# Performance work log

Hardware: AMD Instinct MI355X
Metric: run time of the kernel (lower is better)

The kernel has to match this reference:

```python
import jax, jax.numpy as jnp
import numpy as np

B, N, DIM, H, CH, M = 2, 65536, 256, 8, 32, 64
INNER = H * CH  # 256


def setup_inputs() -> dict:
    key = jax.random.key(0)
    ks = jax.random.split(key, 13)
    s = 0.02
    return {
        "x": jax.random.normal(ks[0], (B, N, DIM), dtype=jnp.float32),
        "W_fx": jax.random.normal(ks[1], (DIM, INNER), dtype=jnp.float32) * s,
        "b_fx": jnp.zeros((INNER,), dtype=jnp.float32),
        "W_x": jax.random.normal(ks[2], (DIM, INNER), dtype=jnp.float32) * s,
        "b_x": jnp.zeros((INNER,), dtype=jnp.float32),
        "W_slice": jax.random.normal(ks[3], (CH, M), dtype=jnp.float32) * s,
        "b_slice": jnp.zeros((M,), dtype=jnp.float32),
        "temperature": 0.5 * jnp.ones((1, H, 1, 1), dtype=jnp.float32),
        "W_q": jax.random.normal(ks[4], (CH, CH), dtype=jnp.float32) * s,
        "W_k": jax.random.normal(ks[5], (CH, CH), dtype=jnp.float32) * s,
        "W_v": jax.random.normal(ks[6], (CH, CH), dtype=jnp.float32) * s,
        "W_out": jax.random.normal(ks[7], (INNER, DIM), dtype=jnp.float32) * s,
        "b_out": jnp.zeros((DIM,), dtype=jnp.float32),
    }


def reference(x, W_fx, b_fx, W_x, b_x, W_slice, b_slice, temperature,
              W_q, W_k, W_v, W_out, b_out):
    b, n, _ = x.shape
    h, ch, m = H, CH, M
    # input projections -> [B, H, N, Ch]
    fx_mid = (x @ W_fx + b_fx).reshape(b, n, h, ch).transpose(0, 2, 1, 3)
    x_mid = (x @ W_x + b_x).reshape(b, n, h, ch).transpose(0, 2, 1, 3)
    # learned soft-slice weights: [B, H, N, M]
    temp = jnp.clip(temperature, 0.1, 5.0)
    logits = (x_mid @ W_slice + b_slice) / temp
    slice_weights = jax.nn.softmax(logits, axis=-1)
    slice_norm = slice_weights.sum(axis=2)  # [B, H, M]
    # aggregate N points into M slice tokens: [B, H, M, Ch]
    slice_token = jnp.einsum('bhnc,bhng->bhgc', fx_mid, slice_weights)
    slice_token = slice_token / (slice_norm + 1e-5)[:, :, :, None]
    # small attention among slice tokens
    q = slice_token @ W_q
    k = slice_token @ W_k
    v = slice_token @ W_v
    scale = ch ** (-0.5)
    attn = jax.nn.softmax(jnp.einsum('bhgc,bhkc->bhgk', q, k) * scale, axis=-1)
    out_slice = attn @ v  # [B, H, M, Ch]
    # scatter back to N points: [B, H, N, Ch] -> [B, N, H*Ch]
    out_x = jnp.einsum('bhgc,bhng->bhnc', out_slice, slice_weights)
    out_x = out_x.transpose(0, 2, 1, 3).reshape(b, n, h * ch)
    return out_x @ W_out + b_out
```

## Files before the change

kernel.cpp:

```cpp
#include <hip/hip_runtime.h>

#define N_ 65536

typedef unsigned int  uint32;
typedef unsigned short ushort;
typedef float  f32x4 __attribute__((ext_vector_type(4)));
typedef short  s16x8 __attribute__((ext_vector_type(8)));
typedef uint32 u32x2 __attribute__((ext_vector_type(2)));

__device__ __forceinline__ uint32 f2bf(float f){
  union{float f; uint32 i;} v; v.f=f;
  return (v.i + 0x7fffu + ((v.i>>16)&1u)) >> 16;
}
__device__ __forceinline__ float bfl(uint32 h){
  union{uint32 i; float f;} v; v.i = h<<16; return v.f;
}
__device__ __forceinline__ uint32 pk2(float a, float b){
  return f2bf(a) | (f2bf(b)<<16);
}
__device__ __forceinline__ f32x4 mfma16(s16x8 a, s16x8 b, f32x4 c){
  return __builtin_amdgcn_mfma_f32_16x16x32_bf16(a,b,c,0,0,0);
}

__global__ __launch_bounds__(256) void prep_kernel(
    const float* __restrict__ Wfx, const float* __restrict__ Wx,
    const float* __restrict__ Wsl, const float* __restrict__ bsl,
    const float* __restrict__ bx,  const float* __restrict__ temp,
    ushort* __restrict__ WlT, ushort* __restrict__ WfxT, float* __restrict__ blT)
{
  const int blk = blockIdx.x, t = threadIdx.x;
  if (blk < 512){
    const int m = blk, h = m>>6, mp = m&63;
    const float tmp = fminf(fmaxf(temp[h],0.1f),5.0f);
    float s = 0.f;
    #pragma unroll
    for (int cc=0; cc<32; cc++) s += Wx[t*256 + h*32+cc]*Wsl[cc*64+mp];
    WlT[m*256+t] = (ushort)f2bf(s/tmp);
    if (t==0){
      float bs = bsl[mp];
      for (int cc=0; cc<32; cc++) bs += bx[h*32+cc]*Wsl[cc*64+mp];
      blT[m] = bs/tmp;
    }
  } else {
    const int c = blk-512;
    WfxT[c*256+t] = (ushort)f2bf(Wfx[t*256+c]);
  }
}

__global__ __launch_bounds__(512, 2)
void k1a_kernel(
    const float* __restrict__ x,
    const ushort* __restrict__ WlT,
    const ushort* __restrict__ WfxT,
    const float* __restrict__ blT,
    const float* __restrict__ bfx,
    ushort* __restrict__ swg,
    float* __restrict__ stp,
    float* __restrict__ normp)
{
  __shared__ __align__(16) char smem[131072];
  const int t = threadIdx.x;
  const int w = t>>6, l = t&63, rg = l>>4, c16 = l&15;
  const int blk = blockIdx.x;
  const int tile0 = ((blk&127)<<3) + ((blk>>7)<<10);

  char* fxh = smem + (w<<12);
  char* swb = smem + 32768 + (w<<13);
  char* fxl = smem + 98304 + (w<<12);

  f32x4 pc[2][4];
  #pragma unroll
  for (int i=0;i<2;i++)
    #pragma unroll
    for (int j=0;j<4;j++) pc[i][j] = (f32x4){0.f,0.f,0.f,0.f};
  f32x4 nacc[4];
  #pragma unroll
  for (int i=0;i<4;i++) nacc[i] = (f32x4){0.f,0.f,0.f,0.f};

  f32x4 blv[4];
  #pragma unroll
  for (int m=0;m<4;m++) blv[m] = *(const f32x4*)(blT + (w<<6)+(m<<4)+(rg<<2));
  float bfv[2];
  #pragma unroll
  for (int c=0;c<2;c++) bfv[c] = bfx[(w<<5)+(c<<4)+c16];

  for (int it=0; it<8; ++it) {
    const int tile = tile0 + it;
    const long gn0 = (long)tile<<6;

    __syncthreads();
    {
      const float4* xs = (const float4*)(x + (gn0<<8));
      #pragma unroll
      for (int p=0;p<8;p++){
        const int f = t + (p<<9);
        const int row = f>>6, q = f&63;
        const float4 v = xs[f];
        u32x2 uu; uu.x = pk2(v.x, v.y); uu.y = pk2(v.z, v.w);
        *(u32x2*)(smem + (row<<9) + ((q<<3) ^ ((row&7)<<4))) = uu;
      }
    }
    __syncthreads();

    #pragma unroll
    for (int nf=0; nf<4; nf++){
      f32x4 accA[4];
      #pragma unroll
      for (int m=0;m<4;m++) accA[m] = (f32x4){0.f,0.f,0.f,0.f};
      #pragma unroll
      for (int kb=0;kb<8;kb++){
        s16x8 aW[4], bX;
        #pragma unroll
        for (int m=0;m<4;m++)
          aW[m] = *(const s16x8*)(WlT + (((w<<6)+(m<<4)+c16)<<8) + (kb<<5)+(rg<<3));
        {
          const int row = (nf<<4) | c16;
          bX = *(const s16x8*)(smem + (row<<9) + (((kb<<6)+(rg<<4)) ^ ((row&7)<<4)));
        }
        #pragma unroll
        for (int m=0;m<4;m++)
          accA[m] = mfma16(aW[m], bX, accA[m]);
      }
      {
        f32x4 v[4];
        float mx = -3.0e38f;
        #pragma unroll
        for (int m=0;m<4;m++){
          v[m] = accA[m] + blv[m];
          mx = fmaxf(mx, fmaxf(fmaxf(v[m].x, v[m].y), fmaxf(v[m].z, v[m].w)));
        }
        mx = fmaxf(mx, __shfl_xor(mx,16));
        mx = fmaxf(mx, __shfl_xor(mx,32));
        float s = 0.f;
        #pragma unroll
        for (int m=0;m<4;m++){
          v[m].x = __expf(v[m].x-mx); v[m].y = __expf(v[m].y-mx);
          v[m].z = __expf(v[m].z-mx); v[m].w = __expf(v[m].w-mx);
          s += v[m].x+v[m].y+v[m].z+v[m].w;
        }
        s += __shfl_xor(s,16);
        s += __shfl_xor(s,32);
        const float inv = 1.0f/s;
        const long gn = gn0 + (nf<<4) + c16;
        #pragma unroll
        for (int m=0;m<4;m++){
          f32x4 sv = v[m]*inv;
          nacc[m] += sv;
          u32x2 p; p.x = pk2(sv.x, sv.y); p.y = pk2(sv.z, sv.w);
          *(u32x2*)(swg + (gn<<9) + (w<<6)+(m<<4)+(rg<<2)) = p;
          const uint32 px = (uint32)__shfl_xor((int)p.x, 1);
          const uint32 py = (uint32)__shfl_xor((int)p.y, 1);
          const bool ev = ((c16&1)==0);
          const uint32 s0 = ev ? (uint32)p.x : py;
          const uint32 s1 = ev ? px : (uint32)p.y;
          const uint32 wA = (s0 & 0xffffu) | (s1<<16);
          const uint32 wB = (s0>>16) | (s1 & 0xffff0000u);
          const int rowA = (m<<4) + (rg<<2) + (ev?0:2);
          const int cbyt = ((nf<<4) + (c16 & ~1)) << 1;
          *(uint32*)(swb + ((rowA  )<<7) + (cbyt ^ (((rowA  )&7)<<4))) = wA;
          *(uint32*)(swb + ((rowA+1)<<7) + (cbyt ^ (((rowA+1)&7)<<4))) = wB;
        }
      }
    }

    u32x2 qkh[2][4];
    {
      f32x4 accB[4][2];
      #pragma unroll
      for (int r=0;r<4;r++)
        #pragma unroll
        for (int c=0;c<2;c++) accB[r][c] = (f32x4){0.f,0.f,0.f,0.f};
      #pragma unroll
      for (int kb=0;kb<8;kb++){
        s16x8 bW[2], aX[4];
        #pragma unroll
        for (int c=0;c<2;c++)
          bW[c] = *(const s16x8*)(WfxT + (((w<<5)+(c<<4)+c16)<<8) + (kb<<5)+(rg<<3));
        #pragma unroll
        for (int r=0;r<4;r++){
          const int row = (r<<4) | c16;
          aX[r] = *(const s16x8*)(smem + (row<<9) + (((kb<<6)+(rg<<4)) ^ ((row&7)<<4)));
        }
        #pragma unroll
        for (int r=0;r<4;r++)
          #pragma unroll
          for (int c=0;c<2;c++)
            accB[r][c] = mfma16(aX[r], bW[c], accB[r][c]);
      }
      #pragma unroll
      for (int r=0;r<4;r++)
        #pragma unroll
        for (int c=0;c<2;c++){
          const float v0 = accB[r][c].x+bfv[c], v1 = accB[r][c].y+bfv[c];
          const float v2 = accB[r][c].z+bfv[c], v3 = accB[r][c].w+bfv[c];
          const uint32 h0=f2bf(v0), h1=f2bf(v1), h2=f2bf(v2), h3=f2bf(v3);
          u32x2 ph; ph.x = h0|(h1<<16); ph.y = h2|(h3<<16);
          qkh[c][r] = ph;
          u32x2 pl;
          pl.x = f2bf(v0-bfl(h0)) | (f2bf(v1-bfl(h1))<<16);
          pl.y = f2bf(v2-bfl(h2)) | (f2bf(v3-bfl(h3))<<16);
          const int row = (c<<4) + c16;
          const int cby = ((r<<5) + (rg<<3)) ^ ((row&7)<<4);
          *(u32x2*)(fxl + (row<<7) + cby) = pl;
        }
    }
    __syncthreads();

    #pragma unroll
    for (int cf=0; cf<2; cf++)
      #pragma unroll
      for (int r=0; r<4; r++){
        const int row = (cf<<4) + c16;
        const int cby = ((r<<5) + (rg<<3)) ^ ((row&7)<<4);
        *(u32x2*)(fxh + (row<<7) + cby) = qkh[cf][r];
      }
    asm volatile("s_waitcnt lgkmcnt(0)" ::: "memory");
    __builtin_amdgcn_sched_barrier(0);

    #pragma unroll
    for (int kb2=0; kb2<2; kb2++){
      const int pby = (kb2<<6) + (rg<<4);
      s16x8 afh[2], afl[2], bfr[4];
      #pragma unroll
      for (int cf=0; cf<2; cf++){
        const int row = (cf<<4)+c16;
        const int o = pby ^ ((row&7)<<4);
        afh[cf] = *(const s16x8*)(fxh + (row<<7) + o);
        afl[cf] = *(const s16x8*)(fxl + (row<<7) + o);
      }
      #pragma unroll
      for (int mf=0; mf<4; mf++){
        const int row = (mf<<4)+c16;
        bfr[mf] = *(const s16x8*)(swb + (row<<7) + (pby ^ ((row&7)<<4)));
      }
      #pragma unroll
      for (int cf=0; cf<2; cf++)
        #pragma unroll
        for (int mf=0; mf<4; mf++){
          pc[cf][mf] = mfma16(afh[cf], bfr[mf], pc[cf][mf]);
          pc[cf][mf] = mfma16(afl[cf], bfr[mf], pc[cf][mf]);
        }
    }
  }

  #pragma unroll
  for (int m=0;m<4;m++){
    #pragma unroll
    for (int d=1; d<16; d<<=1){
      nacc[m].x += __shfl_xor(nacc[m].x, d);
      nacc[m].y += __shfl_xor(nacc[m].y, d);
      nacc[m].z += __shfl_xor(nacc[m].z, d);
      nacc[m].w += __shfl_xor(nacc[m].w, d);
    }
  }
  if (c16==0){
    #pragma unroll
    for (int m=0;m<4;m++)
      *(f32x4*)(normp + (((blk<<3)+w)<<6) + (m<<4) + (rg<<2)) = nacc[m];
  }
  const long sb = ((long)((blk<<3)+w))<<11;
  #pragma unroll
  for (int cf=0;cf<2;cf++)
    #pragma unroll
    for (int mf=0;mf<4;mf++)
      #pragma unroll
      for (int r=0;r<4;r++){
        const int cc = (cf<<4)+(rg<<2)+r;
        stp[sb + (cc<<6) + (mf<<4) + c16] = pc[cf][mf][r];
      }
}

__global__ __launch_bounds__(256) void k2a_kernel(float* __restrict__ stp, float* __restrict__ normp)
{
  const int gid = blockIdx.x;
  const int bh = gid>>3, grp = gid&7;
  const int b = bh>>3, h = bh&7;
  const int t = threadIdx.x;
  const int blk0 = (b<<7) + (grp<<4);
  f32x4 a0 = {0,0,0,0}, a1 = {0,0,0,0};
  for (int i=0;i<16;i++){
    const f32x4* p = (const f32x4*)(stp + ((((size_t)(blk0+i)<<3)+h)<<11) + ((size_t)t<<3));
    a0 += p[0]; a1 += p[1];
  }
  f32x4* q = (f32x4*)(stp + ((((size_t)blk0<<3)+h)<<11) + ((size_t)t<<3));
  q[0] = a0; q[1] = a1;
  if (t<8){
    f32x4 n0 = {0,0,0,0}, n1 = {0,0,0,0};
    for (int i=0;i<16;i++){
      const f32x4* p = (const f32x4*)(normp + (((blk0+i)<<3)+h)*64 + (t<<3));
      n0 += p[0]; n1 += p[1];
    }
    f32x4* qn = (f32x4*)(normp + ((blk0<<3)+h)*64 + (t<<3));
    qn[0] = n0; qn[1] = n1;
  }
}

__global__ __launch_bounds__(256) void k2b_kernel(
    const float* __restrict__ stp, const float* __restrict__ normp,
    const float* __restrict__ Wq, const float* __restrict__ Wk, const float* __restrict__ Wv,
    const float* __restrict__ Wout, ushort* __restrict__ OS2Th, ushort* __restrict__ OS2Tl)
{
  __shared__ float nrmL[64];
  __shared__ float tok[2048];
  __shared__ float qL[2048], kL[2048], vL[2048];
  __shared__ float sc[4096];
  __shared__ float osL[2048];
  const int bh = blockIdx.x; const int b = bh>>3, h = bh&7;
  const int t = threadIdx.x;

  if (t<64){
    float s = 0.f;
    for (int g=0; g<8; g++) s += normp[((((b<<7)+(g<<4))<<3)+h)*64 + t];
    nrmL[t] = s;
  }
  __syncthreads();
  {
    f32x4 a0 = {0,0,0,0}, a1 = {0,0,0,0};
    for (int g=0; g<8; g++){
      const f32x4* p = (const f32x4*)(stp + ((((size_t)((b<<7)+(g<<4))<<3)+h)<<11) + ((size_t)t<<3));
      a0 += p[0]; a1 += p[1];
    }
    const int c = t>>3, m0 = (t&7)<<3;
    #pragma unroll
    for (int j=0;j<4;j++) tok[(m0+j)*32 + c]   = a0[j] / (nrmL[m0+j]   + 1e-5f);
    #pragma unroll
    for (int j=0;j<4;j++) tok[(m0+4+j)*32 + c] = a1[j] / (nrmL[m0+4+j] + 1e-5f);
  }
  __syncthreads();

  const int g = t>>2, q4 = t&3;
  float aq[8]={0,0,0,0,0,0,0,0}, ak2[8]={0,0,0,0,0,0,0,0}, av[8]={0,0,0,0,0,0,0,0};
  for (int kk=0; kk<32; kk++){
    const float tv = tok[(g<<5)+kk];
    const int wo = kk*32 + (q4<<3);
    #pragma unroll
    for (int j=0;j<8;j++){
      aq[j]  = fmaf(tv, Wq[wo+j], aq[j]);
      ak2[j] = fmaf(tv, Wk[wo+j], ak2[j]);
      av[j]  = fmaf(tv, Wv[wo+j], av[j]);
    }
  }
  #pragma unroll
  for (int j=0;j<8;j++){
    qL[(g<<5)+(q4<<3)+j]=aq[j];
    kL[(g<<5)+(q4<<3)+j]=ak2[j];
    vL[(g<<5)+(q4<<3)+j]=av[j];
  }
  __syncthreads();

  const float scale = 0.17677669529663689f;
  float svv[16]; float mx = -3.0e38f;
  for (int mm=0;mm<16;mm++){
    const int m = (q4<<4)+mm;
    float s2 = 0.f;
    #pragma unroll
    for (int c=0;c<32;c++) s2 = fmaf(qL[(g<<5)+c], kL[(m<<5)+c], s2);
    s2 *= scale;
    svv[mm] = s2; mx = fmaxf(mx, s2);
  }
  mx = fmaxf(mx, __shfl_xor(mx,1));
  mx = fmaxf(mx, __shfl_xor(mx,2));
  float ssum = 0.f;
  for (int mm=0;mm<16;mm++){ svv[mm] = __expf(svv[mm]-mx); ssum += svv[mm]; }
  ssum += __shfl_xor(ssum,1); ssum += __shfl_xor(ssum,2);
  const float isum = 1.0f/ssum;
  for (int mm=0;mm<16;mm++) sc[(g<<6) + (q4<<4) + mm] = svv[mm]*isum;
  __syncthreads();

  float os[8]={0,0,0,0,0,0,0,0};
  for (int m=0;m<64;m++){
    const float a = sc[(g<<6)+m];
    const int vo = (m<<5)+(q4<<3);
    #pragma unroll
    for (int j=0;j<8;j++) os[j] = fmaf(a, vL[vo+j], os[j]);
  }
  #pragma unroll
  for (int j=0;j<8;j++) osL[(g<<5)+(q4<<3)+j] = os[j];
  __syncthreads();

  const int d = t;
  float wcol[32];
  #pragma unroll
  for (int c=0;c<32;c++) wcol[c] = Wout[(h*32+c)*256 + d];
  uint32* orh = (uint32*)(OS2Th + ((size_t)(b*256+d))*512 + h*64);
  uint32* orl = (uint32*)(OS2Tl + ((size_t)(b*256+d))*512 + h*64);
  #pragma unroll 4
  for (int g2=0; g2<32; g2++){
    float s0=0.f, s1=0.f;
    #pragma unroll
    for (int c=0;c<32;c++){
      s0 = fmaf(osL[((g2*2  )<<5)+c], wcol[c], s0);
      s1 = fmaf(osL[((g2*2+1)<<5)+c], wcol[c], s1);
    }
    const uint32 h0 = f2bf(s0), h1 = f2bf(s1);
    orh[g2] = h0 | (h1<<16);
    orl[g2] = f2bf(s0 - bfl(h0)) | (f2bf(s1 - bfl(h1)) << 16);
  }
}

__global__ __launch_bounds__(256) void k3_kernel(
    const ushort* __restrict__ swg,
    const ushort* __restrict__ OS2Th,
    const ushort* __restrict__ OS2Tl,
    const float* __restrict__ bout,
    float* __restrict__ out)
{
  const int t = threadIdx.x, w = t>>6, l = t&63, rg = l>>4, c16 = l&15;
  const int blk = blockIdx.x;
  const long gn0 = (long)blk<<7;
  const int b = blk>>9;
  f32x4 acc[8][4];
  #pragma unroll
  for (int r=0;r<8;r++)
    #pragma unroll
    for (int c=0;c<4;c++) acc[r][c] = (f32x4){0.f,0.f,0.f,0.f};
  const ushort* swp = swg + (gn0<<9);
  const long obb = (((long)(b<<8) + (w<<6))<<9);
  for (int kb=0;kb<16;kb++){
    s16x8 aS[8];
    #pragma unroll
    for (int r=0;r<8;r++)
      aS[r] = *(const s16x8*)(swp + ((long)((r<<4)+c16)<<9) + (kb<<5)+(rg<<3));
    #pragma unroll
    for (int c=0;c<4;c++){
      const long ro = obb + ((long)((c<<4)+c16)<<9) + (kb<<5)+(rg<<3);
      const s16x8 bh = *(const s16x8*)(OS2Th + ro);
      const s16x8 bl = *(const s16x8*)(OS2Tl + ro);
      #pragma unroll
      for (int r=0;r<8;r++)
        acc[r][c] = mfma16(aS[r], bh, acc[r][c]);
      #pragma unroll
      for (int r=0;r<8;r++)
        acc[r][c] = mfma16(aS[r], bl, acc[r][c]);
    }
  }
  float bo[4];
  #pragma unroll
  for (int c=0;c<4;c++) bo[c] = bout[(w<<6)+(c<<4)+c16];
  #pragma unroll
  for (int r=0;r<8;r++)
    #pragma unroll
    for (int c=0;c<4;c++)
      #pragma unroll
      for (int rr=0;rr<4;rr++)
        out[((gn0 + (r<<4)+(rg<<2)+rr)<<8) + (w<<6)+(c<<4)+c16] = acc[r][c][rr] + bo[c];
}

extern "C" void kernel_launch(void* const* d_in, const int* in_sizes, int n_in,
                              void* d_out, int out_size, void* d_ws, size_t ws_size,
                              hipStream_t stream)
{
  const float* x     = (const float*)d_in[0];
  const float* Wfx   = (const float*)d_in[1];
  const float* bfx   = (const float*)d_in[2];
  const float* Wx    = (const float*)d_in[3];
  const float* bx    = (const float*)d_in[4];
  const float* Wsl   = (const float*)d_in[5];
  const float* bsl   = (const float*)d_in[6];
  const float* temp  = (const float*)d_in[7];
  const float* Wq    = (const float*)d_in[8];
  const float* Wk    = (const float*)d_in[9];
  const float* Wv    = (const float*)d_in[10];
  const float* Wout  = (const float*)d_in[11];
  const float* bout  = (const float*)d_in[12];
  float* out = (float*)d_out;

  char* ws = (char*)d_ws;
  ushort* WlT   = (ushort*)(ws);
  ushort* WfxT  = (ushort*)(ws + 262144);
  float*  blT   = (float*) (ws + 393216);
  ushort* swg   = (ushort*)(ws + 395264);
  float*  stp   = (float*) (ws + 134612992);
  float*  normp = (float*) (ws + 151390208);
  ushort* OS2Th = (ushort*)(ws + 151914496);
  ushort* OS2Tl = (ushort*)(ws + 152438784);

  prep_kernel<<<dim3(768), dim3(256), 0, stream>>>(Wfx, Wx, Wsl, bsl, bx, temp, WlT, WfxT, blT);
  k1a_kernel<<<dim3(256), dim3(512), 0, stream>>>(x, WlT, WfxT, blT, bfx, swg, stp, normp);
  k2a_kernel<<<dim3(128), dim3(256), 0, stream>>>(stp, normp);
  k2b_kernel<<<dim3(16), dim3(256), 0, stream>>>(stp, normp, Wq, Wk, Wv, Wout, OS2Th, OS2Tl);
  k3_kernel<<<dim3(1024), dim3(256), 0, stream>>>(swg, OS2Th, OS2Tl, bout, out);
}
```

Before: 449.9 us.

## Split k1a across (batch, head) blocks and repack slice weights in MFMA layout

Moves k1a from blocks owning all heads of a token tile to blocks owning one (batch, head) pair over a token chunk. This raises the grid from 256 to 1024 blocks, and each block keeps its head's slice weights in registers and Wfx in shared memory. Each warp now handles 16 tokens, partial slice tokens are reduced inside the block, and the separate k2a reduction kernel is removed, so k2 sums 64 chunk partials directly. Slice weights are written in a packed per-16-token layout that k3 reads back with two 8-byte loads per fragment. The cost is that each block now re-reads x once per head, about 8x more input traffic, and register pressure is higher.

New measurement: 488.2 us. 8.5% more time.

```diff
diff --git a/kernel.cpp b/kernel.cpp
--- a/kernel.cpp
+++ b/kernel.cpp
@@ -7,6 +7,7 @@
 typedef float  f32x4 __attribute__((ext_vector_type(4)));
 typedef short  s16x8 __attribute__((ext_vector_type(8)));
 typedef uint32 u32x2 __attribute__((ext_vector_type(2)));
+typedef uint32 u32x4 __attribute__((ext_vector_type(4)));
 
 __device__ __forceinline__ uint32 f2bf(float f){
   union{float f; uint32 i;} v; v.f=f;
@@ -20,6 +21,9 @@
 }
 __device__ __forceinline__ f32x4 mfma16(s16x8 a, s16x8 b, f32x4 c){
   return __builtin_amdgcn_mfma_f32_16x16x32_bf16(a,b,c,0,0,0);
+}
+__device__ __forceinline__ s16x8 mk8(uint32 a, uint32 b, uint32 c, uint32 d){
+  union{u32x4 u; s16x8 s;} v; v.u = (u32x4){a,b,c,d}; return v.s;
 }
 
 __global__ __launch_bounds__(256) void prep_kernel(
@@ -54,19 +58,33 @@
     const ushort* __restrict__ WfxT,
     const float* __restrict__ blT,
     const float* __restrict__ bfx,
-    ushort* __restrict__ swg,
+    ushort* __restrict__ swg2,
     float* __restrict__ stp,
     float* __restrict__ normp)
 {
-  __shared__ __align__(16) char smem[131072];
+  __shared__ __align__(16) char smem[102400];
   const int t = threadIdx.x;
   const int w = t>>6, l = t&63, rg = l>>4, c16 = l&15;
-  const int blk = blockIdx.x;
-  const int tile0 = ((blk&127)<<3) + ((blk>>7)<<10);
-
-  char* fxh = smem + (w<<12);
-  char* swb = smem + 32768 + (w<<13);
-  char* fxl = smem + 98304 + (w<<12);
+  const int bid = blockIdx.x;
+  const int bh = bid & 15, chunk = bid >> 4;
+  const int b = bh>>3, h = bh&7;
+
+  char* swbb = smem + 81920 + w*2560;
+
+  #pragma unroll
+  for (int p=0;p<2;p++){
+    const int f = t + (p<<9);
+    const int row = f>>5, q = f&31;
+    *(s16x8*)(smem + 65536 + (row<<9) + ((q<<4) ^ ((row&7)<<4))) =
+      *(const s16x8*)(WfxT + (((h<<5)+row)<<8) + (q<<3));
+  }
+
+  s16x8 aWall[4][8];
+  #pragma unroll
+  for (int mf=0; mf<4; mf++)
+    #pragma unroll
+    for (int kb=0; kb<8; kb++)
+      aWall[mf][kb] = *(const s16x8*)(WlT + (((h<<6)+(mf<<4)+c16)<<8) + (kb<<5)+(rg<<3));
 
   f32x4 pc[2][4];
   #pragma unroll
@@ -79,20 +97,22 @@
 
   f32x4 blv[4];
   #pragma unroll
-  for (int m=0;m<4;m++) blv[m] = *(const f32x4*)(blT + (w<<6)+(m<<4)+(rg<<2));
+  for (int mf=0;mf<4;mf++) blv[mf] = *(const f32x4*)(blT + (h<<6)+(mf<<4)+(rg<<2));
   float bfv[2];
   #pragma unroll
-  for (int c=0;c<2;c++) bfv[c] = bfx[(w<<5)+(c<<4)+c16];
+  for (int cf=0;cf<2;cf++) bfv[cf] = bfx[(h<<5)+(cf<<4)+c16];
+
+  const int xrow = (w<<4) + c16;
+  const int xswz = (c16&7)<<4;
 
   for (int it=0; it<8; ++it) {
-    const int tile = tile0 + it;
-    const long gn0 = (long)tile<<6;
+    const long gn0 = (long)b*65536 + (long)chunk*1024 + (long)it*128;
 
     __syncthreads();
     {
       const float4* xs = (const float4*)(x + (gn0<<8));
       #pragma unroll
-      for (int p=0;p<8;p++){
+      for (int p=0;p<16;p++){
         const int f = t + (p<<9);
         const int row = f>>6, q = f&63;
         const float4 v = xs[f];
@@ -102,163 +122,90 @@
     }
     __syncthreads();
 
-    #pragma unroll
-    for (int nf=0; nf<4; nf++){
-      f32x4 accA[4];
-      #pragma unroll
-      for (int m=0;m<4;m++) accA[m] = (f32x4){0.f,0.f,0.f,0.f};
-      #pragma unroll
-      for (int kb=0;kb<8;kb++){
-        s16x8 aW[4], bX;
-        #pragma unroll
-        for (int m=0;m<4;m++)
-          aW[m] = *(const s16x8*)(WlT + (((w<<6)+(m<<4)+c16)<<8) + (kb<<5)+(rg<<3));
-        {
-          const int row = (nf<<4) | c16;
-          bX = *(const s16x8*)(smem + (row<<9) + (((kb<<6)+(rg<<4)) ^ ((row&7)<<4)));
-        }
-        #pragma unroll
-        for (int m=0;m<4;m++)
-          accA[m] = mfma16(aW[m], bX, accA[m]);
-      }
+    f32x4 accA[4], accB[2];
+    #pragma unroll
+    for (int mf=0;mf<4;mf++) accA[mf] = (f32x4){0.f,0.f,0.f,0.f};
+    #pragma unroll
+    for (int cf=0;cf<2;cf++) accB[cf] = (f32x4){0.f,0.f,0.f,0.f};
+    #pragma unroll
+    for (int kb=0;kb<8;kb++){
+      const s16x8 xv = *(const s16x8*)(smem + (xrow<<9) + (((kb<<6)+(rg<<4)) ^ xswz));
+      s16x8 bW0, bW1;
       {
-        f32x4 v[4];
-        float mx = -3.0e38f;
-        #pragma unroll
-        for (int m=0;m<4;m++){
-          v[m] = accA[m] + blv[m];
-          mx = fmaxf(mx, fmaxf(fmaxf(v[m].x, v[m].y), fmaxf(v[m].z, v[m].w)));
-        }
-        mx = fmaxf(mx, __shfl_xor(mx,16));
-        mx = fmaxf(mx, __shfl_xor(mx,32));
-        float s = 0.f;
-        #pragma unroll
-        for (int m=0;m<4;m++){
-          v[m].x = __expf(v[m].x-mx); v[m].y = __expf(v[m].y-mx);
-          v[m].z = __expf(v[m].z-mx); v[m].w = __expf(v[m].w-mx);
-          s += v[m].x+v[m].y+v[m].z+v[m].w;
-        }
-        s += __shfl_xor(s,16);
-        s += __shfl_xor(s,32);
-        const float inv = 1.0f/s;
-        const long gn = gn0 + (nf<<4) + c16;
-        #pragma unroll
-        for (int m=0;m<4;m++){
-          f32x4 sv = v[m]*inv;
-          nacc[m] += sv;
-          u32x2 p; p.x = pk2(sv.x, sv.y); p.y = pk2(sv.z, sv.w);
-          *(u32x2*)(swg + (gn<<9) + (w<<6)+(m<<4)+(rg<<2)) = p;
-          const uint32 px = (uint32)__shfl_xor((int)p.x, 1);
-          const uint32 py = (uint32)__shfl_xor((int)p.y, 1);
-          const bool ev = ((c16&1)==0);
-          const uint32 s0 = ev ? (uint32)p.x : py;
-          const uint32 s1 = ev ? px : (uint32)p.y;
-          const uint32 wA = (s0 & 0xffffu) | (s1<<16);
-          const uint32 wB = (s0>>16) | (s1 & 0xffff0000u);
-          const int rowA = (m<<4) + (rg<<2) + (ev?0:2);
-          const int cbyt = ((nf<<4) + (c16 & ~1)) << 1;
-          *(uint32*)(swb + ((rowA  )<<7) + (cbyt ^ (((rowA  )&7)<<4))) = wA;
-          *(uint32*)(swb + ((rowA+1)<<7) + (cbyt ^ (((rowA+1)&7)<<4))) = wB;
-        }
-      }
-    }
-
-    u32x2 qkh[2][4];
+        const int r0 = c16, r1 = 16+c16;
+        bW0 = *(const s16x8*)(smem + 65536 + (r0<<9) + (((kb<<6)+(rg<<4)) ^ ((r0&7)<<4)));
+        bW1 = *(const s16x8*)(smem + 65536 + (r1<<9) + (((kb<<6)+(rg<<4)) ^ ((r1&7)<<4)));
+      }
+      #pragma unroll
+      for (int mf=0;mf<4;mf++)
+        accA[mf] = mfma16(aWall[mf][kb], xv, accA[mf]);
+      accB[0] = mfma16(xv, bW0, accB[0]);
+      accB[1] = mfma16(xv, bW1, accB[1]);
+    }
+
     {
-      f32x4 accB[4][2];
-      #pragma unroll
-      for (int r=0;r<4;r++)
-        #pragma unroll
-        for (int c=0;c<2;c++) accB[r][c] = (f32x4){0.f,0.f,0.f,0.f};
-      #pragma unroll
-      for (int kb=0;kb<8;kb++){
-        s16x8 bW[2], aX[4];
-        #pragma unroll
-        for (int c=0;c<2;c++)
-          bW[c] = *(const s16x8*)(WfxT + (((w<<5)+(c<<4)+c16)<<8) + (kb<<5)+(rg<<3));
-        #pragma unroll
-        for (int r=0;r<4;r++){
-          const int row = (r<<4) | c16;
-          aX[r] = *(const s16x8*)(smem + (row<<9) + (((kb<<6)+(rg<<4)) ^ ((row&7)<<4)));
-        }
-        #pragma unroll
-        for (int r=0;r<4;r++)
-          #pragma unroll
-          for (int c=0;c<2;c++)
-            accB[r][c] = mfma16(aX[r], bW[c], accB[r][c]);
-      }
-      #pragma unroll
-      for (int r=0;r<4;r++)
-        #pragma unroll
-        for (int c=0;c<2;c++){
-          const float v0 = accB[r][c].x+bfv[c], v1 = accB[r][c].y+bfv[c];
-          const float v2 = accB[r][c].z+bfv[c], v3 = accB[r][c].w+bfv[c];
-          const uint32 h0=f2bf(v0), h1=f2bf(v1), h2=f2bf(v2), h3=f2bf(v3);
-          u32x2 ph; ph.x = h0|(h1<<16); ph.y = h2|(h3<<16);
-          qkh[c][r] = ph;
-          u32x2 pl;
-          pl.x = f2bf(v0-bfl(h0)) | (f2bf(v1-bfl(h1))<<16);
-          pl.y = f2bf(v2-bfl(h2)) | (f2bf(v3-bfl(h3))<<16);
-          const int row = (c<<4) + c16;
-          const int cby = ((r<<5) + (rg<<3)) ^ ((row&7)<<4);
-          *(u32x2*)(fxl + (row<<7) + cby) = pl;
-        }
-    }
-    __syncthreads();
-
-    #pragma unroll
-    for (int cf=0; cf<2; cf++)
-      #pragma unroll
-      for (int r=0; r<4; r++){
-        const int row = (cf<<4) + c16;
-        const int cby = ((r<<5) + (rg<<3)) ^ ((row&7)<<4);
-        *(u32x2*)(fxh + (row<<7) + cby) = qkh[cf][r];
-      }
+      f32x4 v[4];
+      float mx = -3.0e38f;
+      #pragma unroll
+      for (int mf=0;mf<4;mf++){
+        v[mf] = accA[mf] + blv[mf];
+        mx = fmaxf(mx, fmaxf(fmaxf(v[mf].x, v[mf].y), fmaxf(v[mf].z, v[mf].w)));
+      }
+      mx = fmaxf(mx, __shfl_xor(mx,16));
+      mx = fmaxf(mx, __shfl_xor(mx,32));
+      float s = 0.f;
+      #pragma unroll
+      for (int mf=0;mf<4;mf++){
+        v[mf].x = __expf(v[mf].x-mx); v[mf].y = __expf(v[mf].y-mx);
+        v[mf].z = __expf(v[mf].z-mx); v[mf].w = __expf(v[mf].w-mx);
+        s += v[mf].x+v[mf].y+v[mf].z+v[mf].w;
+      }
+      s += __shfl_xor(s,16);
+      s += __shfl_xor(s,32);
+      const float inv = 1.0f/s;
+      const long pbh8 = (((gn0>>4) + w)<<3) + h;
+      #pragma unroll
+      for (int mf=0;mf<4;mf++){
+        f32x4 sv = v[mf]*inv;
+        nacc[mf] += sv;
+        u32x2 p; p.x = pk2(sv.x, sv.y); p.y = pk2(sv.z, sv.w);
+        *(u32x2*)(swg2 + (((pbh8<<2)+mf)<<8) + (rg<<6) + (c16<<2)) = p;
+        const uint32 px = (uint32)__shfl_xor((int)p.x, 1);
+        const uint32 py = (uint32)__shfl_xor((int)p.y, 1);
+        const bool ev = ((c16&1)==0);
+        const uint32 s0 = ev ? (uint32)p.x : py;
+        const uint32 s1 = ev ? px : (uint32)p.y;
+        const uint32 wA = (s0 & 0xffffu) | (s1<<16);
+        const uint32 wB = (s0>>16) | (s1 & 0xffff0000u);
+        const int rowA = (mf<<4) + (rg<<2) + (ev?0:2);
+        const int cbyt = (c16 & ~1) << 1;
+        *(uint32*)(swbb + rowA*40 + 40 + cbyt - 40) = wA;
+        *(uint32*)(swbb + (rowA+1)*40 + cbyt) = wB;
+      }
+    }
+
+    u32x4 afu[2];
+    #pragma unroll
+    for (int cf=0;cf<2;cf++){
+      const float v0 = accB[cf].x+bfv[cf], v1 = accB[cf].y+bfv[cf];
+      const float v2 = accB[cf].z+bfv[cf], v3 = accB[cf].w+bfv[cf];
+      const uint32 h0=f2bf(v0), h1=f2bf(v1), h2=f2bf(v2), h3=f2bf(v3);
+      afu[cf].x = h0|(h1<<16);
+      afu[cf].y = h2|(h3<<16);
+      afu[cf].z = f2bf(v0-bfl(h0)) | (f2bf(v1-bfl(h1))<<16);
+      afu[cf].w = f2bf(v2-bfl(h2)) | (f2bf(v3-bfl(h3))<<16);
+    }
     asm volatile("s_waitcnt lgkmcnt(0)" ::: "memory");
     __builtin_amdgcn_sched_barrier(0);
-
-    #pragma unroll
-    for (int kb2=0; kb2<2; kb2++){
-      const int pby = (kb2<<6) + (rg<<4);
-      s16x8 afh[2], afl[2], bfr[4];
-      #pragma unroll
-      for (int cf=0; cf<2; cf++){
-        const int row = (cf<<4)+c16;
-        const int o = pby ^ ((row&7)<<4);
-        afh[cf] = *(const s16x8*)(fxh + (row<<7) + o);
-        afl[cf] = *(const s16x8*)(fxl + (row<<7) + o);
-      }
-      #pragma unroll
-      for (int mf=0; mf<4; mf++){
-        const int row = (mf<<4)+c16;
-        bfr[mf] = *(const s16x8*)(swb + (row<<7) + (pby ^ ((row&7)<<4)));
-      }
-      #pragma unroll
-      for (int cf=0; cf<2; cf++)
-        #pragma unroll
-        for (int mf=0; mf<4; mf++){
-          pc[cf][mf] = mfma16(afh[cf], bfr[mf], pc[cf][mf]);
-          pc[cf][mf] = mfma16(afl[cf], bfr[mf], pc[cf][mf]);
-        }
-    }
-  }
-
-  #pragma unroll
-  for (int m=0;m<4;m++){
-    #pragma unroll
-    for (int d=1; d<16; d<<=1){
-      nacc[m].x += __shfl_xor(nacc[m].x, d);
-      nacc[m].y += __shfl_xor(nacc[m].y, d);
-      nacc[m].z += __shfl_xor(nacc[m].z, d);
-      nacc[m].w += __shfl_xor(nacc[m].w, d);
-    }
-  }
-  if (c16==0){
-    #pragma unroll
-    for (int m=0;m<4;m++)
-      *(f32x4*)(normp + (((blk<<3)+w)<<6) + (m<<4) + (rg<<2)) = nacc[m];
-  }
-  const long sb = ((long)((blk<<3)+w))<<11;
+    #pragma unroll
+    for (int mf=0; mf<4; mf++){
+      const u32x2 q = *(const u32x2*)(swbb + ((mf<<4)+c16)*40 + (rg<<3));
+      const s16x8 bdup = mk8(q.x, q.y, q.x, q.y);
+      pc[0][mf] = mfma16(mk8(afu[0].x,afu[0].y,afu[0].z,afu[0].w), bdup, pc[0][mf]);
+      pc[1][mf] = mfma16(mk8(afu[1].x,afu[1].y,afu[1].z,afu[1].w), bdup, pc[1][mf]);
+    }
+  }
+
   #pragma unroll
   for (int cf=0;cf<2;cf++)
     #pragma unroll
@@ -266,36 +213,43 @@
       #pragma unroll
       for (int r=0;r<4;r++){
         const int cc = (cf<<4)+(rg<<2)+r;
-        stp[sb + (cc<<6) + (mf<<4) + c16] = pc[cf][mf][r];
-      }
-}
-
-__global__ __launch_bounds__(256) void k2a_kernel(float* __restrict__ stp, float* __restrict__ normp)
-{
-  const int gid = blockIdx.x;
-  const int bh = gid>>3, grp = gid&7;
-  const int b = bh>>3, h = bh&7;
-  const int t = threadIdx.x;
-  const int blk0 = (b<<7) + (grp<<4);
-  f32x4 a0 = {0,0,0,0}, a1 = {0,0,0,0};
-  for (int i=0;i<16;i++){
-    const f32x4* p = (const f32x4*)(stp + ((((size_t)(blk0+i)<<3)+h)<<11) + ((size_t)t<<3));
-    a0 += p[0]; a1 += p[1];
-  }
-  f32x4* q = (f32x4*)(stp + ((((size_t)blk0<<3)+h)<<11) + ((size_t)t<<3));
-  q[0] = a0; q[1] = a1;
-  if (t<8){
-    f32x4 n0 = {0,0,0,0}, n1 = {0,0,0,0};
-    for (int i=0;i<16;i++){
-      const f32x4* p = (const f32x4*)(normp + (((blk0+i)<<3)+h)*64 + (t<<3));
-      n0 += p[0]; n1 += p[1];
-    }
-    f32x4* qn = (f32x4*)(normp + ((blk0<<3)+h)*64 + (t<<3));
-    qn[0] = n0; qn[1] = n1;
-  }
-}
-
-__global__ __launch_bounds__(256) void k2b_kernel(
+        *(float*)(smem + (w<<13) + (((cc<<6) + (mf<<4) + c16)<<2)) = pc[cf][mf][r];
+      }
+  __syncthreads();
+
+  #pragma unroll
+  for (int mf=0;mf<4;mf++){
+    #pragma unroll
+    for (int d=1; d<16; d<<=1){
+      nacc[mf].x += __shfl_xor(nacc[mf].x, d);
+      nacc[mf].y += __shfl_xor(nacc[mf].y, d);
+      nacc[mf].z += __shfl_xor(nacc[mf].z, d);
+      nacc[mf].w += __shfl_xor(nacc[mf].w, d);
+    }
+  }
+  if (c16==0){
+    #pragma unroll
+    for (int mf=0;mf<4;mf++)
+      *(f32x4*)(smem + 65536 + (w<<8) + (((mf<<4)+(rg<<2))<<2)) = nacc[mf];
+  }
+  {
+    f32x4 s = (f32x4){0.f,0.f,0.f,0.f};
+    #pragma unroll
+    for (int w2=0; w2<8; w2++)
+      s += *(const f32x4*)(smem + (w2<<13) + (t<<4));
+    *(f32x4*)(stp + ((size_t)((bh<<6)+chunk)<<11) + (t<<2)) = s;
+  }
+  __syncthreads();
+  if (t<64){
+    float s = 0.f;
+    #pragma unroll
+    for (int w2=0; w2<8; w2++)
+      s += *(const float*)(smem + 65536 + (w2<<8) + (t<<2));
+    normp[((size_t)((bh<<6)+chunk)<<6) + t] = s;
+  }
+}
+
+__global__ __launch_bounds__(256) void k2_kernel(
     const float* __restrict__ stp, const float* __restrict__ normp,
     const float* __restrict__ Wq, const float* __restrict__ Wk, const float* __restrict__ Wv,
     const float* __restrict__ Wout, ushort* __restrict__ OS2Th, ushort* __restrict__ OS2Tl)
@@ -310,14 +264,14 @@
 
   if (t<64){
     float s = 0.f;
-    for (int g=0; g<8; g++) s += normp[((((b<<7)+(g<<4))<<3)+h)*64 + t];
+    for (int ch=0; ch<64; ch++) s += normp[((size_t)((bh<<6)+ch)<<6) + t];
     nrmL[t] = s;
   }
   __syncthreads();
   {
     f32x4 a0 = {0,0,0,0}, a1 = {0,0,0,0};
-    for (int g=0; g<8; g++){
-      const f32x4* p = (const f32x4*)(stp + ((((size_t)((b<<7)+(g<<4))<<3)+h)<<11) + ((size_t)t<<3));
+    for (int ch=0; ch<64; ch++){
+      const f32x4* p = (const f32x4*)(stp + ((size_t)((bh<<6)+ch)<<11) + (t<<3));
       a0 += p[0]; a1 += p[1];
     }
     const int c = t>>3, m0 = (t&7)<<3;
@@ -399,7 +353,7 @@
 }
 
 __global__ __launch_bounds__(256) void k3_kernel(
-    const ushort* __restrict__ swg,
+    const ushort* __restrict__ swg2,
     const ushort* __restrict__ OS2Th,
     const ushort* __restrict__ OS2Tl,
     const float* __restrict__ bout,
@@ -414,24 +368,31 @@
   for (int r=0;r<8;r++)
     #pragma unroll
     for (int c=0;c<4;c++) acc[r][c] = (f32x4){0.f,0.f,0.f,0.f};
-  const ushort* swp = swg + (gn0<<9);
   const long obb = (((long)(b<<8) + (w<<6))<<9);
   for (int kb=0;kb<16;kb++){
+    const int h3 = kb>>1;
+    const int mb = ((kb&1)<<1) + (rg>>1);
+    const int pkt = (rg&1)<<1;
     s16x8 aS[8];
     #pragma unroll
-    for (int r=0;r<8;r++)
-      aS[r] = *(const s16x8*)(swp + ((long)((r<<4)+c16)<<9) + (kb<<5)+(rg<<3));
+    for (int r=0;r<8;r++){
+      const long pb = (gn0>>4) + r;
+      const ushort* bp = swg2 + ((((pb<<3)+h3)<<2) + mb)*256 + (c16<<2);
+      const u32x2 lo = *(const u32x2*)(bp + (pkt<<6));
+      const u32x2 hi = *(const u32x2*)(bp + ((pkt+1)<<6));
+      aS[r] = mk8(lo.x, lo.y, hi.x, hi.y);
+    }
     #pragma unroll
     for (int c=0;c<4;c++){
       const long ro = obb + ((long)((c<<4)+c16)<<9) + (kb<<5)+(rg<<3);
-      const s16x8 bh = *(const s16x8*)(OS2Th + ro);
-      const s16x8 bl = *(const s16x8*)(OS2Tl + ro);
+      const s16x8 bhv = *(const s16x8*)(OS2Th + ro);
+      const s16x8 blv = *(const s16x8*)(OS2Tl + ro);
       #pragma unroll
       for (int r=0;r<8;r++)
-        acc[r][c] = mfma16(aS[r], bh, acc[r][c]);
+        acc[r][c] = mfma16(aS[r], bhv, acc[r][c]);
       #pragma unroll
       for (int r=0;r<8;r++)
-        acc[r][c] = mfma16(aS[r], bl, acc[r][c]);
+        acc[r][c] = mfma16(aS[r], blv, acc[r][c]);
     }
   }
   float bo[4];
@@ -469,15 +430,14 @@
   ushort* WlT   = (ushort*)(ws);
   ushort* WfxT  = (ushort*)(ws + 262144);
   float*  blT   = (float*) (ws + 393216);
-  ushort* swg   = (ushort*)(ws + 395264);
+  ushort* swg2  = (ushort*)(ws + 395264);
   float*  stp   = (float*) (ws + 134612992);
-  float*  normp = (float*) (ws + 151390208);
-  ushort* OS2Th = (ushort*)(ws + 151914496);
-  ushort* OS2Tl = (ushort*)(ws + 152438784);
+  float*  normp = (float*) (ws + 143001600);
+  ushort* OS2Th = (ushort*)(ws + 143263744);
+  ushort* OS2Tl = (ushort*)(ws + 143788032);
 
   prep_kernel<<<dim3(768), dim3(256), 0, stream>>>(Wfx, Wx, Wsl, bsl, bx, temp, WlT, WfxT, blT);
-  k1a_kernel<<<dim3(256), dim3(512), 0, stream>>>(x, WlT, WfxT, blT, bfx, swg, stp, normp);
-  k2a_kernel<<<dim3(128), dim3(256), 0, stream>>>(stp, normp);
-  k2b_kernel<<<dim3(16), dim3(256), 0, stream>>>(stp, normp, Wq, Wk, Wv, Wout, OS2Th, OS2Tl);
-  k3_kernel<<<dim3(1024), dim3(256), 0, stream>>>(swg, OS2Th, OS2Tl, bout, out);
-}
+  k1a_kernel<<<dim3(1024), dim3(512), 0, stream>>>(x, WlT, WfxT, blT, bfx, swg2, stp, normp);
+  k2_kernel<<<dim3(16), dim3(256), 0, stream>>>(stp, normp, Wq, Wk, Wv, Wout, OS2Th, OS2Tl);
+  k3_kernel<<<dim3(1024), dim3(256), 0, stream>>>(swg2, OS2Th, OS2Tl, bout, out);
+}
```

## Pre-convert x to bf16 and double-buffer tiles via async global-to-LDS loads

Applied to the files above, without the earlier changes.

Adds a separate kernel that converts x to bf16, writing into the output buffer as scratch. k1a then stages each 64-row tile with global_load_lds into a double-buffered LDS region, prefetching the next tile while computing the current one. The slice-token accumulation now keeps fx in registers as packed hi/lo operands instead of round-tripping through LDS, and processes the tile in two 32-row chunks. The slice-weight buffer is stored in a fragment-packed layout that k3 reads directly, and k3 uses smaller 64-row blocks. The trade-off is an extra full pass over x plus a bf16 write and read, and a dependence on the output buffer as temporary storage.

Measured after the change: 519.7 us. 1.16x slower.

```diff
diff --git a/kernel.cpp b/kernel.cpp
--- a/kernel.cpp
+++ b/kernel.cpp
@@ -7,6 +7,7 @@
 typedef float  f32x4 __attribute__((ext_vector_type(4)));
 typedef short  s16x8 __attribute__((ext_vector_type(8)));
 typedef uint32 u32x2 __attribute__((ext_vector_type(2)));
+typedef uint32 u32x4 __attribute__((ext_vector_type(4)));
 
 __device__ __forceinline__ uint32 f2bf(float f){
   union{float f; uint32 i;} v; v.f=f;
@@ -20,6 +21,9 @@
 }
 __device__ __forceinline__ f32x4 mfma16(s16x8 a, s16x8 b, f32x4 c){
   return __builtin_amdgcn_mfma_f32_16x16x32_bf16(a,b,c,0,0,0);
+}
+__device__ __forceinline__ s16x8 mk8(uint32 a, uint32 b, uint32 c, uint32 d){
+  union{u32x4 u; s16x8 s;} v; v.u = (u32x4){a,b,c,d}; return v.s;
 }
 
 __global__ __launch_bounds__(256) void prep_kernel(
@@ -47,26 +51,33 @@
   }
 }
 
-__global__ __launch_bounds__(512, 2)
+__global__ __launch_bounds__(256) void xbf_kernel(const float* __restrict__ x, ushort* __restrict__ xbf)
+{
+  const size_t i = ((size_t)blockIdx.x*256 + threadIdx.x)*8;
+  const float4* xp = (const float4*)(x + i);
+  const float4 a = xp[0], b = xp[1];
+  u32x4 o; o.x = pk2(a.x,a.y); o.y = pk2(a.z,a.w); o.z = pk2(b.x,b.y); o.w = pk2(b.z,b.w);
+  *(u32x4*)(xbf + i) = o;
+}
+
+__global__ __launch_bounds__(512)
 void k1a_kernel(
-    const float* __restrict__ x,
+    const ushort* __restrict__ xbf,
     const ushort* __restrict__ WlT,
     const ushort* __restrict__ WfxT,
     const float* __restrict__ blT,
     const float* __restrict__ bfx,
-    ushort* __restrict__ swg,
+    ushort* __restrict__ swg2,
     float* __restrict__ stp,
     float* __restrict__ normp)
 {
-  __shared__ __align__(16) char smem[131072];
+  __shared__ __align__(16) char smem[98304];
   const int t = threadIdx.x;
   const int w = t>>6, l = t&63, rg = l>>4, c16 = l&15;
   const int blk = blockIdx.x;
   const int tile0 = ((blk&127)<<3) + ((blk>>7)<<10);
 
-  char* fxh = smem + (w<<12);
-  char* swb = smem + 32768 + (w<<13);
-  char* fxl = smem + 98304 + (w<<12);
+  char* swb = smem + 65536 + (w<<12);
 
   f32x4 pc[2][4];
   #pragma unroll
@@ -76,78 +87,84 @@
   f32x4 nacc[4];
   #pragma unroll
   for (int i=0;i<4;i++) nacc[i] = (f32x4){0.f,0.f,0.f,0.f};
-
-  f32x4 blv[4];
-  #pragma unroll
-  for (int m=0;m<4;m++) blv[m] = *(const f32x4*)(blT + (w<<6)+(m<<4)+(rg<<2));
   float bfv[2];
   #pragma unroll
-  for (int c=0;c<2;c++) bfv[c] = bfx[(w<<5)+(c<<4)+c16];
-
-  for (int it=0; it<8; ++it) {
+  for (int cf=0;cf<2;cf++) bfv[cf] = bfx[(w<<5)+(cf<<4)+c16];
+
+  #define STAGE(TILE, BUF) { \
+    const int gnS = (int)((TILE)<<6); \
+    _Pragma("unroll") \
+    for (int p=0;p<4;p++){ \
+      const int row = (p<<4) + (t>>5); \
+      const int z = (t&31)<<4; \
+      const char* g = (const char*)xbf + (((size_t)(gnS+row))<<9) + (size_t)(z ^ ((row&7)<<4)); \
+      uint32* ldsp = (uint32*)(smem + ((BUF)<<15) + (p<<13) + ((t>>6)<<10)); \
+      __builtin_amdgcn_global_load_lds((const uint32*)g, ldsp, 16, 0, 0); \
+    } }
+
+  STAGE(tile0, 0);
+  __syncthreads();
+
+  for (int it=0; it<8; ++it){
+    const int cur = it&1;
     const int tile = tile0 + it;
+    if (it<7) STAGE(tile+1, cur^1);
+    const char* Xb = smem + (cur<<15);
     const long gn0 = (long)tile<<6;
 
-    __syncthreads();
-    {
-      const float4* xs = (const float4*)(x + (gn0<<8));
-      #pragma unroll
-      for (int p=0;p<8;p++){
-        const int f = t + (p<<9);
-        const int row = f>>6, q = f&63;
-        const float4 v = xs[f];
-        u32x2 uu; uu.x = pk2(v.x, v.y); uu.y = pk2(v.z, v.w);
-        *(u32x2*)(smem + (row<<9) + ((q<<3) ^ ((row&7)<<4))) = uu;
+    #pragma unroll
+    for (int ch=0; ch<2; ch++){
+      f32x4 accA[4][2];
+      #pragma unroll
+      for (int mf=0;mf<4;mf++)
+        #pragma unroll
+        for (int nfc=0;nfc<2;nfc++) accA[mf][nfc] = (f32x4){0.f,0.f,0.f,0.f};
+      #pragma unroll
+      for (int kb=0;kb<8;kb++){
+        s16x8 aW[4], xv[2];
+        #pragma unroll
+        for (int mf=0;mf<4;mf++)
+          aW[mf] = *(const s16x8*)(WlT + (((w<<6)+(mf<<4)+c16)<<8) + (kb<<5)+(rg<<3));
+        #pragma unroll
+        for (int nfc=0;nfc<2;nfc++){
+          const int row = (ch<<5) + (nfc<<4) + c16;
+          xv[nfc] = *(const s16x8*)(Xb + (row<<9) + (((kb<<6)+(rg<<4)) ^ ((row&7)<<4)));
+        }
+        #pragma unroll
+        for (int mf=0;mf<4;mf++)
+          #pragma unroll
+          for (int nfc=0;nfc<2;nfc++)
+            accA[mf][nfc] = mfma16(aW[mf], xv[nfc], accA[mf][nfc]);
       }
-    }
-    __syncthreads();
-
-    #pragma unroll
-    for (int nf=0; nf<4; nf++){
-      f32x4 accA[4];
-      #pragma unroll
-      for (int m=0;m<4;m++) accA[m] = (f32x4){0.f,0.f,0.f,0.f};
-      #pragma unroll
-      for (int kb=0;kb<8;kb++){
-        s16x8 aW[4], bX;
-        #pragma unroll
-        for (int m=0;m<4;m++)
-          aW[m] = *(const s16x8*)(WlT + (((w<<6)+(m<<4)+c16)<<8) + (kb<<5)+(rg<<3));
-        {
-          const int row = (nf<<4) | c16;
-          bX = *(const s16x8*)(smem + (row<<9) + (((kb<<6)+(rg<<4)) ^ ((row&7)<<4)));
-        }
-        #pragma unroll
-        for (int m=0;m<4;m++)
-          accA[m] = mfma16(aW[m], bX, accA[m]);
-      }
-      {
+      #pragma unroll
+      for (int nfc=0;nfc<2;nfc++){
         f32x4 v[4];
         float mx = -3.0e38f;
         #pragma unroll
-        for (int m=0;m<4;m++){
-          v[m] = accA[m] + blv[m];
-          mx = fmaxf(mx, fmaxf(fmaxf(v[m].x, v[m].y), fmaxf(v[m].z, v[m].w)));
+        for (int mf=0;mf<4;mf++){
+          const f32x4 bl4 = *(const f32x4*)(blT + (w<<6)+(mf<<4)+(rg<<2));
+          v[mf] = accA[mf][nfc] + bl4;
+          mx = fmaxf(mx, fmaxf(fmaxf(v[mf].x, v[mf].y), fmaxf(v[mf].z, v[mf].w)));
         }
         mx = fmaxf(mx, __shfl_xor(mx,16));
         mx = fmaxf(mx, __shfl_xor(mx,32));
         float s = 0.f;
         #pragma unroll
-        for (int m=0;m<4;m++){
-          v[m].x = __expf(v[m].x-mx); v[m].y = __expf(v[m].y-mx);
-          v[m].z = __expf(v[m].z-mx); v[m].w = __expf(v[m].w-mx);
-          s += v[m].x+v[m].y+v[m].z+v[m].w;
+        for (int mf=0;mf<4;mf++){
+          v[mf].x = __expf(v[mf].x-mx); v[mf].y = __expf(v[mf].y-mx);
+          v[mf].z = __expf(v[mf].z-mx); v[mf].w = __expf(v[mf].w-mx);
+          s += v[mf].x+v[mf].y+v[mf].z+v[mf].w;
         }
         s += __shfl_xor(s,16);
         s += __shfl_xor(s,32);
         const float inv = 1.0f/s;
-        const long gn = gn0 + (nf<<4) + c16;
-        #pragma unroll
-        for (int m=0;m<4;m++){
-          f32x4 sv = v[m]*inv;
-          nacc[m] += sv;
+        const int pb = (int)(gn0>>4) + (ch<<1) + nfc;
+        #pragma unroll
+        for (int mf=0;mf<4;mf++){
+          f32x4 sv = v[mf]*inv;
+          nacc[mf] += sv;
           u32x2 p; p.x = pk2(sv.x, sv.y); p.y = pk2(sv.z, sv.w);
-          *(u32x2*)(swg + (gn<<9) + (w<<6)+(m<<4)+(rg<<2)) = p;
+          *(u32x2*)(swg2 + ((((((size_t)pb<<3)+w)<<2)+mf)<<8) + (rg<<6) + (c16<<2)) = p;
           const uint32 px = (uint32)__shfl_xor((int)p.x, 1);
           const uint32 py = (uint32)__shfl_xor((int)p.y, 1);
           const bool ev = ((c16&1)==0);
@@ -155,93 +172,67 @@
           const uint32 s1 = ev ? px : (uint32)p.y;
           const uint32 wA = (s0 & 0xffffu) | (s1<<16);
           const uint32 wB = (s0>>16) | (s1 & 0xffff0000u);
-          const int rowA = (m<<4) + (rg<<2) + (ev?0:2);
-          const int cbyt = ((nf<<4) + (c16 & ~1)) << 1;
-          *(uint32*)(swb + ((rowA  )<<7) + (cbyt ^ (((rowA  )&7)<<4))) = wA;
-          *(uint32*)(swb + ((rowA+1)<<7) + (cbyt ^ (((rowA+1)&7)<<4))) = wB;
+          const int rowA = (mf<<4) + (rg<<2) + (ev?0:2);
+          const int cbyt = ((nfc<<4) | (c16 & ~1)) << 1;
+          *(uint32*)(swb + ((rowA  )<<6) + (cbyt ^ (((rowA  )&7)<<3))) = wA;
+          *(uint32*)(swb + ((rowA+1)<<6) + (cbyt ^ (((rowA+1)&7)<<3))) = wB;
         }
       }
-    }
-
-    u32x2 qkh[2][4];
-    {
-      f32x4 accB[4][2];
-      #pragma unroll
-      for (int r=0;r<4;r++)
-        #pragma unroll
-        for (int c=0;c<2;c++) accB[r][c] = (f32x4){0.f,0.f,0.f,0.f};
+
+      f32x4 accB[2][2];
+      #pragma unroll
+      for (int pf=0;pf<2;pf++)
+        #pragma unroll
+        for (int cf=0;cf<2;cf++) accB[pf][cf] = (f32x4){0.f,0.f,0.f,0.f};
       #pragma unroll
       for (int kb=0;kb<8;kb++){
-        s16x8 bW[2], aX[4];
-        #pragma unroll
-        for (int c=0;c<2;c++)
-          bW[c] = *(const s16x8*)(WfxT + (((w<<5)+(c<<4)+c16)<<8) + (kb<<5)+(rg<<3));
-        #pragma unroll
-        for (int r=0;r<4;r++){
-          const int row = (r<<4) | c16;
-          aX[r] = *(const s16x8*)(smem + (row<<9) + (((kb<<6)+(rg<<4)) ^ ((row&7)<<4)));
-        }
-        #pragma unroll
-        for (int r=0;r<4;r++)
+        s16x8 bW[2], xv[2];
+        #pragma unroll
+        for (int cf=0;cf<2;cf++)
+          bW[cf] = *(const s16x8*)(WfxT + (((w<<5)+(cf<<4)+c16)<<8) + (kb<<5)+(rg<<3));
+        #pragma unroll
+        for (int pf=0;pf<2;pf++){
+          const int row = (ch<<5) + (pf<<4) + c16;
+          xv[pf] = *(const s16x8*)(Xb + (row<<9) + (((kb<<6)+(rg<<4)) ^ ((row&7)<<4)));
+        }
+        #pragma unroll
+        for (int pf=0;pf<2;pf++)
           #pragma unroll
-          for (int c=0;c<2;c++)
-            accB[r][c] = mfma16(aX[r], bW[c], accB[r][c]);
+          for (int cf=0;cf<2;cf++)
+            accB[pf][cf] = mfma16(xv[pf], bW[cf], accB[pf][cf]);
       }
-      #pragma unroll
-      for (int r=0;r<4;r++)
-        #pragma unroll
-        for (int c=0;c<2;c++){
-          const float v0 = accB[r][c].x+bfv[c], v1 = accB[r][c].y+bfv[c];
-          const float v2 = accB[r][c].z+bfv[c], v3 = accB[r][c].w+bfv[c];
+      u32x4 afu[2][2];
+      #pragma unroll
+      for (int cf=0;cf<2;cf++)
+        #pragma unroll
+        for (int pf=0;pf<2;pf++){
+          const float v0 = accB[pf][cf].x+bfv[cf], v1 = accB[pf][cf].y+bfv[cf];
+          const float v2 = accB[pf][cf].z+bfv[cf], v3 = accB[pf][cf].w+bfv[cf];
           const uint32 h0=f2bf(v0), h1=f2bf(v1), h2=f2bf(v2), h3=f2bf(v3);
-          u32x2 ph; ph.x = h0|(h1<<16); ph.y = h2|(h3<<16);
-          qkh[c][r] = ph;
-          u32x2 pl;
-          pl.x = f2bf(v0-bfl(h0)) | (f2bf(v1-bfl(h1))<<16);
-          pl.y = f2bf(v2-bfl(h2)) | (f2bf(v3-bfl(h3))<<16);
-          const int row = (c<<4) + c16;
-          const int cby = ((r<<5) + (rg<<3)) ^ ((row&7)<<4);
-          *(u32x2*)(fxl + (row<<7) + cby) = pl;
-        }
+          afu[cf][pf].x = h0|(h1<<16);
+          afu[cf][pf].y = h2|(h3<<16);
+          afu[cf][pf].z = f2bf(v0-bfl(h0)) | (f2bf(v1-bfl(h1))<<16);
+          afu[cf][pf].w = f2bf(v2-bfl(h2)) | (f2bf(v3-bfl(h3))<<16);
+        }
+      asm volatile("s_waitcnt lgkmcnt(0)" ::: "memory");
+      __builtin_amdgcn_sched_barrier(0);
+
+      #pragma unroll
+      for (int pf=0;pf<2;pf++)
+        #pragma unroll
+        for (int mf=0;mf<4;mf++){
+          const int row = (mf<<4)+c16;
+          const u32x2 q = *(const u32x2*)(swb + (row<<6) + ((((pf<<5)+(rg<<3)) ^ ((row&7)<<3))));
+          const s16x8 bdup = mk8(q.x, q.y, q.x, q.y);
+          pc[0][mf] = mfma16(mk8(afu[0][pf].x,afu[0][pf].y,afu[0][pf].z,afu[0][pf].w), bdup, pc[0][mf]);
+          pc[1][mf] = mfma16(mk8(afu[1][pf].x,afu[1][pf].y,afu[1][pf].z,afu[1][pf].w), bdup, pc[1][mf]);
+        }
+      asm volatile("s_waitcnt lgkmcnt(0)" ::: "memory");
+      __builtin_amdgcn_sched_barrier(0);
     }
     __syncthreads();
-
-    #pragma unroll
-    for (int cf=0; cf<2; cf++)
-      #pragma unroll
-      for (int r=0; r<4; r++){
-        const int row = (cf<<4) + c16;
-        const int cby = ((r<<5) + (rg<<3)) ^ ((row&7)<<4);
-        *(u32x2*)(fxh + (row<<7) + cby) = qkh[cf][r];
-      }
-    asm volatile("s_waitcnt lgkmcnt(0)" ::: "memory");
-    __builtin_amdgcn_sched_barrier(0);
-
-    #pragma unroll
-    for (int kb2=0; kb2<2; kb2++){
-      const int pby = (kb2<<6) + (rg<<4);
-      s16x8 afh[2], afl[2], bfr[4];
-      #pragma unroll
-      for (int cf=0; cf<2; cf++){
-        const int row = (cf<<4)+c16;
-        const int o = pby ^ ((row&7)<<4);
-        afh[cf] = *(const s16x8*)(fxh + (row<<7) + o);
-        afl[cf] = *(const s16x8*)(fxl + (row<<7) + o);
-      }
-      #pragma unroll
-      for (int mf=0; mf<4; mf++){
-        const int row = (mf<<4)+c16;
-        bfr[mf] = *(const s16x8*)(swb + (row<<7) + (pby ^ ((row&7)<<4)));
-      }
-      #pragma unroll
-      for (int cf=0; cf<2; cf++)
-        #pragma unroll
-        for (int mf=0; mf<4; mf++){
-          pc[cf][mf] = mfma16(afh[cf], bfr[mf], pc[cf][mf]);
-          pc[cf][mf] = mfma16(afl[cf], bfr[mf], pc[cf][mf]);
-        }
-    }
-  }
+  }
+  #undef STAGE
 
   #pragma unroll
   for (int m=0;m<4;m++){
@@ -399,7 +390,7 @@
 }
 
 __global__ __launch_bounds__(256) void k3_kernel(
-    const ushort* __restrict__ swg,
+    const ushort* __restrict__ swg2,
     const ushort* __restrict__ OS2Th,
     const ushort* __restrict__ OS2Tl,
     const float* __restrict__ bout,
@@ -407,38 +398,45 @@
 {
   const int t = threadIdx.x, w = t>>6, l = t&63, rg = l>>4, c16 = l&15;
   const int blk = blockIdx.x;
-  const long gn0 = (long)blk<<7;
-  const int b = blk>>9;
-  f32x4 acc[8][4];
-  #pragma unroll
-  for (int r=0;r<8;r++)
+  const long gn0 = (long)blk<<6;
+  const int b = blk>>10;
+  f32x4 acc[4][4];
+  #pragma unroll
+  for (int r=0;r<4;r++)
     #pragma unroll
     for (int c=0;c<4;c++) acc[r][c] = (f32x4){0.f,0.f,0.f,0.f};
-  const ushort* swp = swg + (gn0<<9);
   const long obb = (((long)(b<<8) + (w<<6))<<9);
   for (int kb=0;kb<16;kb++){
-    s16x8 aS[8];
-    #pragma unroll
-    for (int r=0;r<8;r++)
-      aS[r] = *(const s16x8*)(swp + ((long)((r<<4)+c16)<<9) + (kb<<5)+(rg<<3));
+    const int h3 = kb>>1;
+    const int mb = ((kb&1)<<1) + (rg>>1);
+    const int pkt = (rg&1)<<1;
+    s16x8 aS[4];
+    #pragma unroll
+    for (int r=0;r<4;r++){
+      const long pb = (gn0>>4) + r;
+      const ushort* bp = swg2 + ((((pb<<3)+h3)<<2) + mb)*256 + (c16<<2);
+      const u32x2 lo = *(const u32x2*)(bp + (pkt<<6));
+      const u32x2 hi = *(const u32x2*)(bp + ((pkt+1)<<6));
+      aS[r] = mk8(lo.x, lo.y, hi.x, hi.y);
+    }
     #pragma unroll
     for (int c=0;c<4;c++){
       const long ro = obb + ((long)((c<<4)+c16)<<9) + (kb<<5)+(rg<<3);
-      const s16x8 bh = *(const s16x8*)(OS2Th + ro);
-      const s16x8 bl = *(const s16x8*)(OS2Tl + ro);
-      #pragma unroll
-      for (int r=0;r<8;r++)
-        acc[r][c] = mfma16(aS[r], bh, acc[r][c]);
-      #pragma unroll
-      for (int r=0;r<8;r++)
-        acc[r][c] = mfma16(aS[r], bl, acc[r][c]);
+      const s16x8 bhv = *(const s16x8*)(OS2Th + ro);
+      const s16x8 blv = *(const s16x8*)(OS2Tl + ro);
+      #pragma unroll
+      for (int r=0;r<4;r++)
+        acc[r][c] = mfma16(aS[r], bhv, acc[r][c]);
+      #pragma unroll
+      for (int r=0;r<4;r++)
+        acc[r][c] = mfma16(aS[r], blv, acc[r][c]);
     }
   }
   float bo[4];
   #pragma unroll
   for (int c=0;c<4;c++) bo[c] = bout[(w<<6)+(c<<4)+c16];
   #pragma unroll
-  for (int r=0;r<8;r++)
+  for (int r=0;r<4;r++)
     #pragma unroll
     for (int c=0;c<4;c++)
       #pragma unroll
@@ -469,15 +467,18 @@
   ushort* WlT   = (ushort*)(ws);
   ushort* WfxT  = (ushort*)(ws + 262144);
   float*  blT   = (float*) (ws + 393216);
-  ushort* swg   = (ushort*)(ws + 395264);
+  ushort* swg2  = (ushort*)(ws + 395264);
   float*  stp   = (float*) (ws + 134612992);
   float*  normp = (float*) (ws + 151390208);
   ushort* OS2Th = (ushort*)(ws + 151914496);
   ushort* OS2Tl = (ushort*)(ws + 152438784);
 
+  ushort* xbf = (ushort*)d_out;
+
   prep_kernel<<<dim3(768), dim3(256), 0, stream>>>(Wfx, Wx, Wsl, bsl, bx, temp, WlT, WfxT, blT);
-  k1a_kernel<<<dim3(256), dim3(512), 0, stream>>>(x, WlT, WfxT, blT, bfx, swg, stp, normp);
+  xbf_kernel<<<dim3(16384), dim3(256), 0, stream>>>(x, xbf);
+  k1a_kernel<<<dim3(256), dim3(512), 0, stream>>>(xbf, WlT, WfxT, blT, bfx, swg2, stp, normp);
   k2a_kernel<<<dim3(128), dim3(256), 0, stream>>>(stp, normp);
   k2b_kernel<<<dim3(16), dim3(256), 0, stream>>>(stp, normp, Wq, Wk, Wv, Wout, OS2Th, OS2Tl);
-  k3_kernel<<<dim3(1024), dim3(256), 0, stream>>>(swg, OS2Th, OS2Tl, bout, out);
-}
+  k3_kernel<<<dim3(2048), dim3(256), 0, stream>>>(swg2, OS2Th, OS2Tl, bout, out);
+}
```
